# Performance work log

Measured on AMD Instinct MI355X. Metric: run time of the kernel, lower is better.

The kernel has to match this reference:

```python
import jax, jax.numpy as jnp
import numpy as np

EPS = 1e-6
SLIDING_WINDOW = 512
ROPE_BASE = 10000.0  # rope_local_base_freq for sliding_attention layers


def _rms_norm(x, w=None):
    # Gemma-style RMSNorm computed in fp32 then cast back
    xf = x.astype(jnp.float32)
    out = xf * jax.lax.rsqrt(jnp.mean(xf * xf, axis=-1, keepdims=True) + EPS)
    if w is not None:
        out = out * w.astype(jnp.float32)
    return out.astype(x.dtype)


def _rotate_half(x):
    x1, x2 = jnp.split(x, 2, axis=-1)
    return jnp.concatenate((-x2, x1), axis=-1)


def setup_inputs() -> dict:
    key = jax.random.key(0)
    ks = jax.random.split(key, 6)
    B, S, H, NH, NKV, D = 1, 4096, 2048, 8, 2, 256
    hidden_states = jax.random.normal(ks[0], (B, S, H), dtype=jnp.float32)
    w_q = jax.random.normal(ks[1], (H, NH * D), dtype=jnp.float32) * 0.02
    w_k = jax.random.normal(ks[2], (H, NKV * D), dtype=jnp.float32) * 0.02
    w_v = jax.random.normal(ks[3], (H, NKV * D), dtype=jnp.float32) * 0.02
    w_o = jax.random.normal(ks[4], (NH * D, H), dtype=jnp.float32) * 0.02
    q_norm_w = jnp.ones((D,), dtype=jnp.float32)
    k_norm_w = jnp.ones((D,), dtype=jnp.float32)
    # RoPE tables (local base freq, sliding layer)
    inv_freq = 1.0 / (ROPE_BASE ** (jnp.arange(0, D, 2, dtype=jnp.float32) / D))
    pos = jnp.arange(S, dtype=jnp.float32)
    freqs = pos[:, None] * inv_freq[None, :]          # [S, D/2]
    emb = jnp.concatenate((freqs, freqs), axis=-1)    # [S, D]
    cos = jnp.broadcast_to(jnp.cos(emb)[None], (B, S, D)).astype(jnp.float32)
    sin = jnp.broadcast_to(jnp.sin(emb)[None], (B, S, D)).astype(jnp.float32)
    return {"hidden_states": hidden_states, "w_q": w_q, "w_k": w_k, "w_v": w_v,
            "w_o": w_o, "q_norm_w": q_norm_w, "k_norm_w": k_norm_w,
            "cos": cos, "sin": sin}


def reference(hidden_states, w_q, w_k, w_v, w_o, q_norm_w, k_norm_w, cos, sin):
    B, S, _ = hidden_states.shape
    D = cos.shape[-1]
    NH = w_q.shape[1] // D
    NKV = w_k.shape[1] // D
    G = NH // NKV

    # projections -> [B, S, heads, D], per-head RMSNorm (Gemma3n-style)
    q = _rms_norm((hidden_states @ w_q).reshape(B, S, NH, D), q_norm_w)
    k = _rms_norm((hidden_states @ w_k).reshape(B, S, NKV, D), k_norm_w)
    v = _rms_norm((hidden_states @ w_v).reshape(B, S, NKV, D))  # v_norm: no scale

    q = q.transpose(0, 2, 1, 3)  # [B, NH, S, D]
    k = k.transpose(0, 2, 1, 3)  # [B, NKV, S, D]
    v = v.transpose(0, 2, 1, 3)

    # RoPE, cos/sin unsqueezed over the head dim
    c = cos[:, None, :, :]
    s = sin[:, None, :, :]
    q = q * c + _rotate_half(q) * s
    k = k * c + _rotate_half(k) * s

    # GQA: repeat KV heads
    k = jnp.repeat(k, G, axis=1)  # [B, NH, S, D]
    v = jnp.repeat(v, G, axis=1)

    # attention, scaling = 1.0 (q_norm replaces 1/sqrt(d) in this family)
    scores = jnp.einsum('bhqd,bhkd->bhqk', q, k)

    # causal + sliding-window mask
    i = jnp.arange(S)[:, None]
    j = jnp.arange(S)[None, :]
    mask = (j <= i) & ((i - j) < SLIDING_WINDOW)
    scores = jnp.where(mask[None, None], scores, jnp.finfo(scores.dtype).min)

    attn = jax.nn.softmax(scores.astype(jnp.float32), axis=-1).astype(q.dtype)
    out = jnp.einsum('bhqk,bhkd->bhqd', attn, v)
    out = out.transpose(0, 2, 1, 3).reshape(B, S, NH * D)
    return out @ w_o
```

## Files before the change

kernel.cpp:

```cpp
#include <hip/hip_runtime.h>
#include <hip/hip_bf16.h>

#define S_LEN 4096
#define HDIM  2048
#define NHQ   8
#define NKVH  2
#define DHEAD 256
#define WIN   512
#define NQKV  3072

typedef __hip_bfloat16 bf16_t;
using fragAB = __attribute__((ext_vector_type(8))) short;
using fragC  = __attribute__((ext_vector_type(4))) float;

typedef unsigned int u32;
typedef const __attribute__((address_space(1))) u32* gas_ptr;
typedef __attribute__((address_space(3))) u32* las_ptr;

__device__ __forceinline__ void async_copy16(const void* g, void* l) {
  __builtin_amdgcn_global_load_lds((gas_ptr)g, (las_ptr)l, 16, 0, 0);
}

#define NEG_BIG (-3.0e38f)

__device__ __forceinline__ void split2(float x, bf16_t& hi, bf16_t& lo) {
  bf16_t h = __float2bfloat16(x);
  hi = h;
  lo = __float2bfloat16(x - (float)h);
}

__global__ __launch_bounds__(256) void split_f32(
    const float* __restrict__ in, bf16_t* __restrict__ hi,
    bf16_t* __restrict__ lo, int n) {
  int i = (blockIdx.x * 256 + threadIdx.x) * 4;
  if (i >= n) return;
  float4 v = *(const float4*)(in + i);
  split2(v.x, hi[i + 0], lo[i + 0]);
  split2(v.y, hi[i + 1], lo[i + 1]);
  split2(v.z, hi[i + 2], lo[i + 2]);
  split2(v.w, hi[i + 3], lo[i + 3]);
}

__global__ __launch_bounds__(256) void transpose_cvt(
    const float* __restrict__ in, bf16_t* __restrict__ out, int R, int C) {
  __shared__ bf16_t tile[32][33];
  int c0 = blockIdx.x * 32, r0 = blockIdx.y * 32;
  int tx = threadIdx.x & 31, ty = threadIdx.x >> 5;
#pragma unroll
  for (int i = 0; i < 4; ++i)
    tile[ty + i * 8][tx] = __float2bfloat16(in[(size_t)(r0 + ty + i * 8) * C + c0 + tx]);
  __syncthreads();
#pragma unroll
  for (int i = 0; i < 4; ++i)
    out[(size_t)(c0 + ty + i * 8) * R + r0 + tx] = tile[tx][ty + i * 8];
}

__global__ __launch_bounds__(256) void transpose_split_fused(
    const float* __restrict__ wq, const float* __restrict__ wk,
    const float* __restrict__ wv, bf16_t* __restrict__ hiT,
    bf16_t* __restrict__ loT) {
  __shared__ bf16_t th[32][33];
  __shared__ bf16_t tl[32][33];
  int oc = blockIdx.x * 32;
  int r0 = blockIdx.y * 32;
  const float* src; int C, c0;
  if (oc < 2048)      { src = wq; C = 2048; c0 = oc; }
  else if (oc < 2560) { src = wk; C = 512;  c0 = oc - 2048; }
  else                { src = wv; C = 512;  c0 = oc - 2560; }
  int tx = threadIdx.x & 31, ty = threadIdx.x >> 5;
#pragma unroll
  for (int i = 0; i < 4; ++i) {
    float x = src[(size_t)(r0 + ty + i * 8) * C + c0 + tx];
    bf16_t h, l; split2(x, h, l);
    th[ty + i * 8][tx] = h;
    tl[ty + i * 8][tx] = l;
  }
  __syncthreads();
#pragma unroll
  for (int i = 0; i < 4; ++i) {
    hiT[(size_t)(oc + ty + i * 8) * HDIM + r0 + tx] = th[tx][ty + i * 8];
    loT[(size_t)(oc + ty + i * 8) * HDIM + r0 + tx] = tl[tx][ty + i * 8];
  }
}

#define VMCNT_(n) asm volatile("s_waitcnt vmcnt(" #n ")" ::: "memory")
#define VMCNT(n) VMCNT_(n)
#define BARRIER()                     \
  {                                   \
    asm volatile("" ::: "memory");    \
    __builtin_amdgcn_s_barrier();     \
    asm volatile("" ::: "memory");    \
  }

#define MFMA_(a, b, c) __builtin_amdgcn_mfma_f32_16x16x32_bf16(a, b, c, 0, 0, 0)

#define OFF_AH 0
#define OFF_AL 16384
#define OFF_BH 32768
#define OFF_BL 45056
#define BUFSZ  57344

#define LOADB()                                                   \
  _Pragma("unroll")                                               \
  for (int j = 0; j < 3; ++j) {                                   \
    const char* bp_ = bufc + (wn + j * 16 + l16) * 64 + rdq;      \
    bh[j] = *(const fragAB*)(bp_ + OFF_BH);                       \
    bl[j] = *(const fragAB*)(bp_ + OFF_BL);                       \
  }

struct ARegs { fragAB ah0, al0, ah1, al1; };

__device__ __forceinline__ void lda_split(ARegs& r, const char* bufc, int wm,
                                          int p, int l16, int rdq) {
  const char* a0 = bufc + (wm + (2 * p) * 16 + l16) * 64 + rdq;
  const char* a1 = a0 + 16 * 64;
  r.ah0 = *(const fragAB*)(a0 + OFF_AH);
  r.al0 = *(const fragAB*)(a0 + OFF_AL);
  r.ah1 = *(const fragAB*)(a1 + OFF_AH);
  r.al1 = *(const fragAB*)(a1 + OFF_AL);
}

__device__ __forceinline__ void mfma_split(fragC (&acc)[8][3], const ARegs& r,
                                           const fragAB (&bh)[3],
                                           const fragAB (&bl)[3], int p) {
  __builtin_amdgcn_s_setprio(1);
#pragma unroll
  for (int j = 0; j < 3; ++j) {
    acc[2 * p][j]     = MFMA_(r.al0, bh[j], acc[2 * p][j]);
    acc[2 * p + 1][j] = MFMA_(r.al1, bh[j], acc[2 * p + 1][j]);
  }
#pragma unroll
  for (int j = 0; j < 3; ++j) {
    acc[2 * p][j]     = MFMA_(r.ah0, bl[j], acc[2 * p][j]);
    acc[2 * p + 1][j] = MFMA_(r.ah1, bl[j], acc[2 * p + 1][j]);
  }
#pragma unroll
  for (int j = 0; j < 3; ++j) {
    acc[2 * p][j]     = MFMA_(r.ah0, bh[j], acc[2 * p][j]);
    acc[2 * p + 1][j] = MFMA_(r.ah1, bh[j], acc[2 * p + 1][j]);
  }
  __builtin_amdgcn_s_setprio(0);
}

#define SPLIT_STEP()                        \
  {                                         \
    LOADB();                                \
    lda_split(r0, bufc, wm, 0, l16, rdq);   \
    lda_split(r1, bufc, wm, 1, l16, rdq);   \
    mfma_split(acc, r0, bh, bl, 0);         \
    lda_split(r0, bufc, wm, 2, l16, rdq);   \
    mfma_split(acc, r1, bh, bl, 1);         \
    lda_split(r1, bufc, wm, 3, l16, rdq);   \
    mfma_split(acc, r0, bh, bl, 2);         \
    mfma_split(acc, r1, bh, bl, 3);         \
  }

__global__ __launch_bounds__(512, 2) void gemm_split2(
    const bf16_t* __restrict__ Ah, const bf16_t* __restrict__ Al,
    const bf16_t* __restrict__ Bh, const bf16_t* __restrict__ Bl,
    float* __restrict__ C, int M, int N, int K) {
  __shared__ __align__(16) char lds[2 * BUFSZ];
  const int t = threadIdx.x;
  const int wave = t >> 6, lane = t & 63;
  const int quad = lane >> 4, l16 = lane & 15;
  const int m0 = blockIdx.y * 256, n0 = blockIdx.x * 192;
  const int wm = (wave >> 2) * 128, wn = (wave & 3) * 48;
  const int rdq = (quad ^ ((l16 >> 1) & 3)) * 16;

  const size_t laneOff =
      (size_t)(lane >> 2) * K * 2 + 16 * ((lane & 3) ^ ((lane >> 3) & 3));

  const char* gsrc[7];
  int ldsOff[7];
#pragma unroll
  for (int pos = 0; pos < 3; ++pos) {
    int c = wave + 8 * pos;
    if (c < 12) {
      gsrc[pos]   = (const char*)Bh + (size_t)(n0 + 16 * c) * K * 2 + laneOff;
      ldsOff[pos] = OFF_BH + c * 1024;
    } else {
      gsrc[pos]   = (const char*)Bl + (size_t)(n0 + 16 * (c - 12)) * K * 2 + laneOff;
      ldsOff[pos] = OFF_BL + (c - 12) * 1024;
    }
  }
#pragma unroll
  for (int p = 0; p < 4; ++p) {
    int sub = wave & 3;
    int R0 = ((sub >> 1) & 1) * 128 + 32 * p + (sub & 1) * 16;
    const char* base = (const char*)(wave < 4 ? Ah : Al);
    gsrc[3 + p]   = base + (size_t)(m0 + R0) * K * 2 + laneOff;
    ldsOff[3 + p] = (wave < 4 ? OFF_AH : OFF_AL) + R0 * 64;
  }

  fragC zero4 = {0.f, 0.f, 0.f, 0.f};
  fragC acc[8][3];
#pragma unroll
  for (int i = 0; i < 8; ++i)
#pragma unroll
    for (int j = 0; j < 3; ++j) acc[i][j] = zero4;

  char* ldsc = (char*)lds;
#pragma unroll
  for (int ps = 0; ps < 7; ++ps) async_copy16(gsrc[ps], ldsc + ldsOff[ps]);
#pragma unroll
  for (int ps = 0; ps < 7; ++ps) gsrc[ps] += 64;

  fragAB bh[3], bl[3];
  ARegs r0, r1;
  int cur = 0;
  const int NS = K / 32;
  for (int it = 0; it < NS - 1; ++it) {
    const char* bufc = ldsc + cur * BUFSZ;
    char* nb = ldsc + (cur ^ 1) * BUFSZ;
    VMCNT(0); BARRIER();
#pragma unroll
    for (int ps = 0; ps < 7; ++ps) async_copy16(gsrc[ps], nb + ldsOff[ps]);
#pragma unroll
    for (int ps = 0; ps < 7; ++ps) gsrc[ps] += 64;
    SPLIT_STEP();
    cur ^= 1;
  }
  {
    const char* bufc = ldsc + cur * BUFSZ;
    VMCNT(0); BARRIER();
    SPLIT_STEP();
  }

#pragma unroll
  for (int i = 0; i < 8; ++i)
#pragma unroll
    for (int j = 0; j < 3; ++j)
#pragma unroll
      for (int r = 0; r < 4; ++r) {
        int row = m0 + wm + i * 16 + quad * 4 + r;
        int col = n0 + wn + j * 16 + l16;
        C[(size_t)row * N + col] = acc[i][j][r];
      }
}

#define BT_OFF_A 0
#define BT_OFF_B 32768
#define BT_BUFSZ 49152

struct ARegs2 { fragAB a[2][2]; };

__device__ __forceinline__ void lda_bt(ARegs2& r, const char* bufc, int wm,
                                       int p, int l16, int quad, int rx) {
#pragma unroll
  for (int u = 0; u < 2; ++u)
#pragma unroll
    for (int ks = 0; ks < 2; ++ks)
      r.a[u][ks] = *(const fragAB*)(bufc + BT_OFF_A +
                                    (wm + (2 * p + u) * 16 + l16) * 128 +
                                    (((ks * 4 + quad) ^ rx) * 16));
}

__device__ __forceinline__ void mfma_bt(fragC (&acc)[8][2], const ARegs2& r,
                                        const fragAB (&b)[2][2], int p) {
  __builtin_amdgcn_s_setprio(1);
#pragma unroll
  for (int ks = 0; ks < 2; ++ks)
#pragma unroll
    for (int j = 0; j < 2; ++j) {
      acc[2 * p][j]     = MFMA_(r.a[0][ks], b[j][ks], acc[2 * p][j]);
      acc[2 * p + 1][j] = MFMA_(r.a[1][ks], b[j][ks], acc[2 * p + 1][j]);
    }
  __builtin_amdgcn_s_setprio(0);
}

#define BT_LOADB()                                                        \
  _Pragma("unroll")                                                       \
  for (int j = 0; j < 2; ++j)                                             \
  _Pragma("unroll")                                                       \
    for (int ks = 0; ks < 2; ++ks)                                        \
      bfr[j][ks] = *(const fragAB*)(bufc + BT_OFF_B +                     \
                                    (wn + j * 16 + l16) * 128 +           \
                                    (((ks * 4 + quad) ^ rx) * 16));

#define BT_STEP()                                 \
  {                                               \
    BT_LOADB();                                   \
    lda_bt(r0, bufc, wm, 0, l16, quad, rx);       \
    lda_bt(r1, bufc, wm, 1, l16, quad, rx);       \
    mfma_bt(acc, r0, bfr, 0);                     \
    lda_bt(r0, bufc, wm, 2, l16, quad, rx);       \
    mfma_bt(acc, r1, bfr, 1);                     \
    lda_bt(r1, bufc, wm, 3, l16, quad, rx);       \
    mfma_bt(acc, r0, bfr, 2);                     \
    mfma_bt(acc, r1, bfr, 3);                     \
  }

__global__ __launch_bounds__(512, 2) void gemm_bt2(
    const bf16_t* __restrict__ A, const bf16_t* __restrict__ Bt,
    float* __restrict__ C, int M, int N, int K) {
  __shared__ __align__(16) char lds[2 * BT_BUFSZ];
  const int t = threadIdx.x;
  const int wave = t >> 6, lane = t & 63;
  const int quad = lane >> 4, l16 = lane & 15;
  const int m0 = blockIdx.y * 256, n0 = blockIdx.x * 128;
  const int wm = (wave >> 2) * 128, wn = (wave & 3) * 32;
  const int rx = l16 & 7;

  const size_t laneOff =
      (size_t)(lane >> 3) * K * 2 + 16 * ((lane & 7) ^ ((lane >> 3) & 7));

  const char* gsrc[6];
  int ldsOff[6];
#pragma unroll
  for (int pos = 0; pos < 2; ++pos) {
    int c = wave + 8 * pos;
    gsrc[pos]   = (const char*)Bt + (size_t)(n0 + 8 * c) * K * 2 + laneOff;
    ldsOff[pos] = BT_OFF_B + c * 1024;
  }
#pragma unroll
  for (int p = 0; p < 4; ++p) {
    int R0 = (wave >> 2) * 128 + 32 * p + (wave & 3) * 8;
    gsrc[2 + p]   = (const char*)A + (size_t)(m0 + R0) * K * 2 + laneOff;
    ldsOff[2 + p] = BT_OFF_A + R0 * 128;
  }

  fragC zero4 = {0.f, 0.f, 0.f, 0.f};
  fragC acc[8][2];
#pragma unroll
  for (int i = 0; i < 8; ++i)
#pragma unroll
    for (int j = 0; j < 2; ++j) acc[i][j] = zero4;

  char* ldsc = (char*)lds;
#pragma unroll
  for (int ps = 0; ps < 6; ++ps) async_copy16(gsrc[ps], ldsc + ldsOff[ps]);
#pragma unroll
  for (int ps = 0; ps < 6; ++ps) gsrc[ps] += 128;

  fragAB bfr[2][2];
  ARegs2 r0, r1;
  int cur = 0;
  const int NS = K / 64;
  for (int it = 0; it < NS - 1; ++it) {
    const char* bufc = ldsc + cur * BT_BUFSZ;
    char* nb = ldsc + (cur ^ 1) * BT_BUFSZ;
    VMCNT(0); BARRIER();
#pragma unroll
    for (int ps = 0; ps < 6; ++ps) async_copy16(gsrc[ps], nb + ldsOff[ps]);
#pragma unroll
    for (int ps = 0; ps < 6; ++ps) gsrc[ps] += 128;
    BT_STEP();
    cur ^= 1;
  }
  {
    const char* bufc = ldsc + cur * BT_BUFSZ;
    VMCNT(0); BARRIER();
    BT_STEP();
  }

#pragma unroll
  for (int i = 0; i < 8; ++i)
#pragma unroll
    for (int j = 0; j < 2; ++j)
#pragma unroll
      for (int r = 0; r < 4; ++r) {
        int row = m0 + wm + i * 16 + quad * 4 + r;
        int col = n0 + wn + j * 16 + l16;
        C[(size_t)row * N + col] = acc[i][j][r];
      }
}

__global__ __launch_bounds__(256) void rmsnorm_rope_split_qk(
    const float* __restrict__ proj, const float* __restrict__ qnw,
    const float* __restrict__ knw, const float* __restrict__ cosb,
    const float* __restrict__ sinb, bf16_t* __restrict__ qhi,
    bf16_t* __restrict__ qlo, bf16_t* __restrict__ khi,
    bf16_t* __restrict__ klo) {
  int s = blockIdx.x, hb = blockIdx.y, d = threadIdx.x;
  const float* w; bf16_t* oh; bf16_t* ol; int inOff, outStride, oBase;
  if (hb < NHQ) {
    w = qnw; oh = qhi; ol = qlo;
    inOff = hb * DHEAD; outStride = NHQ * DHEAD; oBase = hb * DHEAD;
  } else {
    int hk = hb - NHQ;
    w = knw; oh = khi; ol = klo;
    inOff = NHQ * DHEAD + hk * DHEAD; outStride = NKVH * DHEAD; oBase = hk * DHEAD;
  }
  float x = proj[(size_t)s * NQKV + inOff + d];
  float ss = x * x;
  ss += __shfl_xor(ss, 1);  ss += __shfl_xor(ss, 2);  ss += __shfl_xor(ss, 4);
  ss += __shfl_xor(ss, 8);  ss += __shfl_xor(ss, 16); ss += __shfl_xor(ss, 32);
  __shared__ float part[4];
  __shared__ float xs[DHEAD];
  if ((threadIdx.x & 63) == 0) part[threadIdx.x >> 6] = ss;
  __syncthreads();
  float tot = part[0] + part[1] + part[2] + part[3];
  float r = rsqrtf(tot * (1.0f / DHEAD) + 1e-6f);
  float xn = x * r * w[d];
  xs[d] = xn;
  __syncthreads();
  float other = xs[(d + 128) & 255];
  float rot = (d < 128) ? -other : other;
  float y = xn * cosb[(size_t)s * DHEAD + d] + rot * sinb[(size_t)s * DHEAD + d];
  bf16_t h2, l2; split2(y, h2, l2);
  size_t oidx = (size_t)s * outStride + oBase + d;
  oh[oidx] = h2;
  ol[oidx] = l2;
}

__global__ __launch_bounds__(256) void rmsnorm_vT2(
    const float* __restrict__ proj, bf16_t* __restrict__ vt, int inOff) {
  __shared__ float rs_[32];
  __shared__ bf16_t tile[32][33];
  int s0 = blockIdx.x * 32, hh = blockIdx.y;
  const float* base = proj + (size_t)s0 * NQKV + inOff + hh * DHEAD;
  int t = threadIdx.x;
  int sl = t >> 3, c8 = t & 7;
  const float4* rowp = (const float4*)(base + (size_t)sl * NQKV + c8 * 32);
  float ss = 0.f;
#pragma unroll
  for (int i = 0; i < 8; ++i) {
    float4 v = rowp[i];
    ss += v.x * v.x + v.y * v.y + v.z * v.z + v.w * v.w;
  }
  ss += __shfl_xor(ss, 1); ss += __shfl_xor(ss, 2); ss += __shfl_xor(ss, 4);
  if (c8 == 0) rs_[sl] = rsqrtf(ss * (1.0f / DHEAD) + 1e-6f);
  __syncthreads();
  int tx = t & 31, ty = t >> 5;
#pragma unroll
  for (int ch = 0; ch < 8; ++ch) {
#pragma unroll
    for (int i = 0; i < 4; ++i) {
      int s_ = ty + i * 8;
      float x = base[(size_t)s_ * NQKV + ch * 32 + tx];
      tile[s_][tx] = __float2bfloat16(x * rs_[s_]);
    }
    __syncthreads();
#pragma unroll
    for (int i = 0; i < 4; ++i) {
      int dl = ty + i * 8;
      vt[((size_t)hh * DHEAD + ch * 32 + dl) * S_LEN + s0 + tx] = tile[tx][dl];
    }
    __syncthreads();
  }
}

__global__ __launch_bounds__(512, 2) void attn_split(
    const bf16_t* __restrict__ Qhi, const bf16_t* __restrict__ Qlo,
    const bf16_t* __restrict__ Khi, const bf16_t* __restrict__ Klo,
    const bf16_t* __restrict__ Vt, bf16_t* __restrict__ Aout) {
  const int h = blockIdx.y;
  const int qb = blockIdx.x * 128;
  const int wave = threadIdx.x >> 6, lane = threadIdx.x & 63;
  const int quad = lane >> 4, l16 = lane & 15;
  const int qw = qb + wave * 16;
  const int kv = h >> 2;
  const bf16_t* Qh_ = Qhi + h * DHEAD;
  const bf16_t* Ql_ = Qlo + h * DHEAD;
  const bf16_t* Kh_ = Khi + kv * DHEAD;
  const bf16_t* Kl_ = Klo + kv * DHEAD;
  const bf16_t* Vh_ = Vt + (size_t)kv * DHEAD * S_LEN;

  __shared__ __align__(16) bf16_t KshH[2][32 * 256];
  __shared__ __align__(16) bf16_t KshL[2][32 * 256];
  __shared__ __align__(16) bf16_t Vsh[2][256 * 32];
  __shared__ __align__(16) bf16_t Plds[8][16 * 32];

  fragAB qfh[8], qfl[8];
#pragma unroll
  for (int c = 0; c < 8; ++c) {
    size_t off = (size_t)(qw + l16) * (NHQ * DHEAD) + c * 32 + quad * 8;
    qfh[c] = *(const fragAB*)(Qh_ + off);
    qfl[c] = *(const fragAB*)(Ql_ + off);
  }

  int kRow[2], kCol[2], vRow[2], vCol[2];
#pragma unroll
  for (int i = 0; i < 2; ++i) {
    int ci = i * 512 + threadIdx.x;
    kRow[i] = ci >> 5;
    kCol[i] = ((ci & 31) ^ (kRow[i] & 31)) * 8;
    vRow[i] = ci >> 2;
    vCol[i] = ((ci & 3) ^ (vRow[i] & 3)) * 8;
  }

#define ASTAGE(buf, kb_)                                                     \
  _Pragma("unroll")                                                          \
  for (int i = 0; i < 2; ++i) {                                              \
    size_t dst = (size_t)(i * 512 + threadIdx.x) * 16;                       \
    size_t koff = (size_t)((kb_) + kRow[i]) * (NKVH * DHEAD) + kCol[i];      \
    async_copy16(Kh_ + koff, (char*)KshH[buf] + dst);                        \
    async_copy16(Kl_ + koff, (char*)KshL[buf] + dst);                        \
    async_copy16(Vh_ + (size_t)vRow[i] * S_LEN + (kb_) + vCol[i],            \
                 (char*)Vsh[buf] + dst);                                     \
  }

  fragC zero4 = {0.f, 0.f, 0.f, 0.f};
  fragC o_acc[16];
#pragma unroll
  for (int c = 0; c < 16; ++c) o_acc[c] = zero4;
  float m_run[4] = {NEG_BIG, NEG_BIG, NEG_BIG, NEG_BIG};
  float l_run[4] = {0.f, 0.f, 0.f, 0.f};
  const float LOG2E = 1.4426950408889634f;

  int k_lo = qb - (WIN - 1);
  if (k_lo < 0) k_lo = 0;
  k_lo &= ~31;

  ASTAGE(0, k_lo);
  int cur = 0;

  for (int kb = k_lo; kb < qb + 128; kb += 32) {
    VMCNT(0); BARRIER();
    if (kb + 32 < qb + 128) {
      int nbuf = cur ^ 1;
      ASTAGE(nbuf, kb + 32);
    }
    const char* KH = (const char*)KshH[cur];
    const char* KL = (const char*)KshL[cur];
    const char* VB = (const char*)Vsh[cur];

    fragC s[2] = {zero4, zero4};
#pragma unroll
    for (int c = 0; c < 8; ++c) {
      int j = c * 4 + quad;
#pragma unroll
      for (int g = 0; g < 2; ++g) {
        int row = g * 16 + l16;
        int off = (row * 32 + (j ^ (row & 31))) * 16;
        fragAB kh = *(const fragAB*)(KH + off);
        fragAB kl = *(const fragAB*)(KL + off);
        s[g] = __builtin_amdgcn_mfma_f32_16x16x32_bf16(qfl[c], kh, s[g], 0, 0, 0);
        s[g] = __builtin_amdgcn_mfma_f32_16x16x32_bf16(qfh[c], kl, s[g], 0, 0, 0);
        s[g] = __builtin_amdgcn_mfma_f32_16x16x32_bf16(qfh[c], kh, s[g], 0, 0, 0);
      }
    }

    float p[2][4], alpha[4];
#pragma unroll
    for (int r = 0; r < 4; ++r) {
      int qi = qw + quad * 4 + r;
      bool vld[2];
      float mx = NEG_BIG;
#pragma unroll
      for (int g = 0; g < 2; ++g) {
        int ki = kb + g * 16 + l16;
        vld[g] = (ki <= qi) && (qi - ki < WIN);
        mx = fmaxf(mx, vld[g] ? s[g][r] : NEG_BIG);
      }
      mx = fmaxf(mx, __shfl_xor(mx, 1));
      mx = fmaxf(mx, __shfl_xor(mx, 2));
      mx = fmaxf(mx, __shfl_xor(mx, 4));
      mx = fmaxf(mx, __shfl_xor(mx, 8));
      float mn = fmaxf(m_run[r], mx);
      float a  = exp2f(fmaxf(m_run[r] - mn, -80.f) * LOG2E);
      float rs = 0.f;
#pragma unroll
      for (int g = 0; g < 2; ++g) {
        float e = vld[g] ? exp2f(fmaxf(s[g][r] - mn, -80.f) * LOG2E) : 0.f;
        p[g][r] = e;
        rs += e;
      }
      rs += __shfl_xor(rs, 1);
      rs += __shfl_xor(rs, 2);
      rs += __shfl_xor(rs, 4);
      rs += __shfl_xor(rs, 8);
      l_run[r] = l_run[r] * a + rs;
      m_run[r] = mn;
      alpha[r] = a;
    }
#pragma unroll
    for (int c = 0; c < 16; ++c)
#pragma unroll
      for (int r = 0; r < 4; ++r) o_acc[c][r] *= alpha[r];

    bf16_t* Pw = Plds[wave];
#pragma unroll
    for (int r = 0; r < 4; ++r)
#pragma unroll
      for (int g = 0; g < 2; ++g)
        Pw[(quad * 4 + r) * 32 + g * 16 + l16] = __float2bfloat16(p[g][r]);
    fragAB pf = *(const fragAB*)((const char*)Pw + l16 * 64 + quad * 16);

#pragma unroll
    for (int c = 0; c < 16; ++c) {
      int d = c * 16 + l16;
      int offv = (d * 4 + (quad ^ (d & 3))) * 16;
      fragAB vf = *(const fragAB*)(VB + offv);
      o_acc[c] = __builtin_amdgcn_mfma_f32_16x16x32_bf16(pf, vf, o_acc[c], 0, 0, 0);
    }
    cur ^= 1;
  }

  float inv_l[4];
#pragma unroll
  for (int r = 0; r < 4; ++r) inv_l[r] = 1.0f / l_run[r];
#pragma unroll
  for (int c = 0; c < 16; ++c)
#pragma unroll
    for (int r = 0; r < 4; ++r) {
      int row = qw + quad * 4 + r;
      int col = h * DHEAD + c * 16 + l16;
      Aout[(size_t)row * (NHQ * DHEAD) + col] = __float2bfloat16(o_acc[c][r] * inv_l[r]);
    }
#undef ASTAGE
}

extern "C" void kernel_launch(void* const* d_in, const int* in_sizes, int n_in,
                              void* d_out, int out_size, void* d_ws, size_t ws_size,
                              hipStream_t stream) {
  const float* hid  = (const float*)d_in[0];
  const float* w_q  = (const float*)d_in[1];
  const float* w_k  = (const float*)d_in[2];
  const float* w_v  = (const float*)d_in[3];
  const float* w_o  = (const float*)d_in[4];
  const float* qnw  = (const float*)d_in[5];
  const float* knw  = (const float*)d_in[6];
  const float* cosb = (const float*)d_in[7];
  const float* sinb = (const float*)d_in[8];
  float* outp = (float*)d_out;

  const size_t M1 = 1048576;
  bf16_t* w = (bf16_t*)d_ws;
  bf16_t* hidh  = w;
  bf16_t* qh    = w;
  bf16_t* hidl  = w + 8 * M1;
  bf16_t* ql    = w + 8 * M1;
  bf16_t* wTh   = w + 16 * M1;
  bf16_t* kh    = w + 16 * M1;
  bf16_t* kl    = w + 18 * M1;
  bf16_t* vt    = w + 20 * M1;
  bf16_t* wTl   = w + 22 * M1;
  bf16_t* woT   = w + 22 * M1;
  float*  projqkv = (float*)(w + 28 * M1);
  bf16_t* aout  = w + 28 * M1;

  split_f32<<<(S_LEN * HDIM) / 1024, 256, 0, stream>>>(hid, hidh, hidl, S_LEN * HDIM);
  transpose_split_fused<<<dim3(NQKV / 32, HDIM / 32), 256, 0, stream>>>(
      w_q, w_k, w_v, wTh, wTl);

  gemm_split2<<<dim3(NQKV / 192, S_LEN / 256), 512, 0, stream>>>(
      hidh, hidl, wTh, wTl, projqkv, S_LEN, NQKV, HDIM);

  rmsnorm_rope_split_qk<<<dim3(S_LEN, NHQ + NKVH), 256, 0, stream>>>(
      projqkv, qnw, knw, cosb, sinb, qh, ql, kh, kl);
  rmsnorm_vT2<<<dim3(S_LEN / 32, NKVH), 256, 0, stream>>>(
      projqkv, vt, NHQ * DHEAD + NKVH * DHEAD);

  transpose_cvt<<<dim3(HDIM / 32, (NHQ * DHEAD) / 32), 256, 0, stream>>>(w_o, woT, NHQ * DHEAD, HDIM);

  attn_split<<<dim3(S_LEN / 128, NHQ), 512, 0, stream>>>(qh, ql, kh, kl, vt, aout);

  gemm_bt2<<<dim3(HDIM / 128, S_LEN / 256), 512, 0, stream>>>(
      aout, woT, outp, S_LEN, HDIM, NHQ * DHEAD);
}
```

Before: 408.7 us.

## Remap block indices for XCD-aware locality and raise wave priority around MFMA loops

Both GEMM kernels and the attention kernel now remap the linear block id so that consecutive blocks, which are dispatched round-robin across the 8 XCDs, land on related tiles. This is meant to improve L2 reuse of shared A/B tiles and of K/V windows within each XCD. The attention kernel also raises wave priority with s_setprio during the QK and PV MFMA sections, to interleave matrix work better with the softmax code of other waves. The hardcoded grid decompositions assume the fixed grid sizes (16x16 and 32x8).

```diff
diff --git a/kernel.cpp b/kernel.cpp
--- a/kernel.cpp
+++ b/kernel.cpp
@@ -163,7 +163,10 @@
   const int t = threadIdx.x;
   const int wave = t >> 6, lane = t & 63;
   const int quad = lane >> 4, l16 = lane & 15;
-  const int m0 = blockIdx.y * 256, n0 = blockIdx.x * 192;
+  const int g = blockIdx.y * 16 + blockIdx.x;
+  const int lby = (g & 7) * 2 + ((g >> 3) >> 4);
+  const int lbx = (g >> 3) & 15;
+  const int m0 = lby * 256, n0 = lbx * 192;
   const int wm = (wave >> 2) * 128, wn = (wave & 3) * 48;
   const int rdq = (quad ^ ((l16 >> 1) & 3)) * 16;
 
@@ -297,7 +300,10 @@
   const int t = threadIdx.x;
   const int wave = t >> 6, lane = t & 63;
   const int quad = lane >> 4, l16 = lane & 15;
-  const int m0 = blockIdx.y * 256, n0 = blockIdx.x * 128;
+  const int g = blockIdx.y * 16 + blockIdx.x;
+  const int lby = (g & 7) * 2 + ((g >> 3) >> 4);
+  const int lbx = (g >> 3) & 15;
+  const int m0 = lby * 256, n0 = lbx * 128;
   const int wm = (wave >> 2) * 128, wn = (wave & 3) * 32;
   const int rx = l16 & 7;
 
@@ -444,8 +450,10 @@
     const bf16_t* __restrict__ Qhi, const bf16_t* __restrict__ Qlo,
     const bf16_t* __restrict__ Khi, const bf16_t* __restrict__ Klo,
     const bf16_t* __restrict__ Vt, bf16_t* __restrict__ Aout) {
-  const int h = blockIdx.y;
-  const int qb = blockIdx.x * 128;
+  const int g = blockIdx.y * 32 + blockIdx.x;
+  const int lbx = (g & 7) * 4 + ((g >> 3) & 3);
+  const int h = g >> 5;
+  const int qb = lbx * 128;
   const int wave = threadIdx.x >> 6, lane = threadIdx.x & 63;
   const int quad = lane >> 4, l16 = lane & 15;
   const int qw = qb + wave * 16;
@@ -516,20 +524,22 @@
     const char* VB = (const char*)Vsh[cur];
 
     fragC s[2] = {zero4, zero4};
+    __builtin_amdgcn_s_setprio(1);
 #pragma unroll
     for (int c = 0; c < 8; ++c) {
       int j = c * 4 + quad;
 #pragma unroll
-      for (int g = 0; g < 2; ++g) {
-        int row = g * 16 + l16;
+      for (int gg = 0; gg < 2; ++gg) {
+        int row = gg * 16 + l16;
         int off = (row * 32 + (j ^ (row & 31))) * 16;
         fragAB kh = *(const fragAB*)(KH + off);
         fragAB kl = *(const fragAB*)(KL + off);
-        s[g] = __builtin_amdgcn_mfma_f32_16x16x32_bf16(qfl[c], kh, s[g], 0, 0, 0);
-        s[g] = __builtin_amdgcn_mfma_f32_16x16x32_bf16(qfh[c], kl, s[g], 0, 0, 0);
-        s[g] = __builtin_amdgcn_mfma_f32_16x16x32_bf16(qfh[c], kh, s[g], 0, 0, 0);
+        s[gg] = __builtin_amdgcn_mfma_f32_16x16x32_bf16(qfl[c], kh, s[gg], 0, 0, 0);
+        s[gg] = __builtin_amdgcn_mfma_f32_16x16x32_bf16(qfh[c], kl, s[gg], 0, 0, 0);
+        s[gg] = __builtin_amdgcn_mfma_f32_16x16x32_bf16(qfh[c], kh, s[gg], 0, 0, 0);
       }
     }
+    __builtin_amdgcn_s_setprio(0);
 
     float p[2][4], alpha[4];
 #pragma unroll
@@ -538,10 +548,10 @@
       bool vld[2];
       float mx = NEG_BIG;
 #pragma unroll
-      for (int g = 0; g < 2; ++g) {
-        int ki = kb + g * 16 + l16;
-        vld[g] = (ki <= qi) && (qi - ki < WIN);
-        mx = fmaxf(mx, vld[g] ? s[g][r] : NEG_BIG);
+      for (int gg = 0; gg < 2; ++gg) {
+        int ki = kb + gg * 16 + l16;
+        vld[gg] = (ki <= qi) && (qi - ki < WIN);
+        mx = fmaxf(mx, vld[gg] ? s[gg][r] : NEG_BIG);
       }
       mx = fmaxf(mx, __shfl_xor(mx, 1));
       mx = fmaxf(mx, __shfl_xor(mx, 2));
@@ -551,9 +561,9 @@
       float a  = exp2f(fmaxf(m_run[r] - mn, -80.f) * LOG2E);
       float rs = 0.f;
 #pragma unroll
-      for (int g = 0; g < 2; ++g) {
-        float e = vld[g] ? exp2f(fmaxf(s[g][r] - mn, -80.f) * LOG2E) : 0.f;
-        p[g][r] = e;
+      for (int gg = 0; gg < 2; ++gg) {
+        float e = vld[gg] ? exp2f(fmaxf(s[gg][r] - mn, -80.f) * LOG2E) : 0.f;
+        p[gg][r] = e;
         rs += e;
       }
       rs += __shfl_xor(rs, 1);
@@ -573,10 +583,11 @@
 #pragma unroll
     for (int r = 0; r < 4; ++r)
 #pragma unroll
-      for (int g = 0; g < 2; ++g)
-        Pw[(quad * 4 + r) * 32 + g * 16 + l16] = __float2bfloat16(p[g][r]);
+      for (int gg = 0; gg < 2; ++gg)
+        Pw[(quad * 4 + r) * 32 + gg * 16 + l16] = __float2bfloat16(p[gg][r]);
     fragAB pf = *(const fragAB*)((const char*)Pw + l16 * 64 + quad * 16);
 
+    __builtin_amdgcn_s_setprio(1);
 #pragma unroll
     for (int c = 0; c < 16; ++c) {
       int d = c * 16 + l16;
@@ -584,6 +595,7 @@
       fragAB vf = *(const fragAB*)(VB + offv);
       o_acc[c] = __builtin_amdgcn_mfma_f32_16x16x32_bf16(pf, vf, o_acc[c], 0, 0, 0);
     }
+    __builtin_amdgcn_s_setprio(0);
     cur ^= 1;
   }
 
@@ -641,8 +653,8 @@
       projqkv, qnw, knw, cosb, sinb, qh, ql, kh, kl);
   rmsnorm_vT2<<<dim3(S_LEN / 32, NKVH), 256, 0, stream>>>(
       projqkv, vt, NHQ * DHEAD + NKVH * DHEAD);
-
-  transpose_cvt<<<dim3(HDIM / 32, (NHQ * DHEAD) / 32), 256, 0, stream>>>(w_o, woT, NHQ * DHEAD, HDIM);
+  transpose_cvt<<<dim3(HDIM / 32, (NHQ * DHEAD) / 32), 256, 0, stream>>>(
+      w_o, woT, NHQ * DHEAD, HDIM);
 
   attn_split<<<dim3(S_LEN / 128, NHQ), 512, 0, stream>>>(qh, ql, kh, kl, vt, aout);
 
```

Result: no change. 404.0 us (-1.2%).
